# Kernel optimization log

Measured on AMD Instinct MI355X. Metric: run time of the kernel, lower is better.

Reference implementation:

```python
import jax, jax.numpy as jnp
import numpy as np

H = W = 32
C = 512
RED = 16


def make_gus(v=1.5):
    # gus[p=(i,k), x, y] = exp(-((x-i)^2+(y-k)^2)/(2 v^2)) / (2 pi v^2), normalized per p.
    idx = np.arange(H, dtype=np.float64)
    d2 = (idx[:, None] - idx[None, :]) ** 2          # [center, coord]
    g1 = np.exp(-d2 / (2.0 * v * v))                  # separable factor
    g = np.einsum('ix,ky->ikxy', g1, g1) / (2.0 * np.pi * v * v)
    g = g / g.sum(axis=(2, 3), keepdims=True)         # per-position normalization
    return jnp.asarray(g.reshape(H * W, H, W), dtype=jnp.float32)


def setup_inputs() -> dict:
    key = jax.random.key(0)
    ks = jax.random.split(key, 6)
    b = 16
    return {
        'x': jax.random.normal(ks[0], (b, C, H, W), dtype=jnp.float32),
        'se_w1': jax.random.normal(ks[1], (C // RED, C), dtype=jnp.float32) * 0.02,
        'se_b1': jnp.zeros((C // RED,), dtype=jnp.float32),
        'se_w2': jax.random.normal(ks[2], (C, C // RED), dtype=jnp.float32) * 0.02,
        'se_b2': jnp.zeros((C,), dtype=jnp.float32),
        'down_w': jax.random.normal(ks[3], (C, 2 * C), dtype=jnp.float32) * 0.02,
        'gus': make_gus(1.5),
    }


def _patches3(img, h, w):
    # img: [b, c, h+2, w+2] -> [b, c, h, w, 9] (3x3 neighborhoods, row-major dy*3+dx)
    ps = [img[:, :, dy:dy + h, dx:dx + w] for dy in range(3) for dx in range(3)]
    return jnp.stack(ps, axis=-1)


def reference(x, se_w1, se_b1, se_w2, se_b2, down_w, gus):
    b, c, h, w = x.shape
    # --- SELayer ---
    s = x.mean(axis=(2, 3))                                   # [b, c]
    y = jax.nn.relu(s @ se_w1.T + se_b1)                       # [b, c/16]
    y = jax.nn.sigmoid(y @ se_w2.T + se_b2)                    # [b, c]
    out32 = x * y[:, :, None, None]
    # --- gaussian-weighted global pooling per output position ---
    # g[b, p, ch] = sum_{y,x} gus[p,y,x] * out32[b,ch,y,x]; then torch's view(c,h,w)
    gus_out = jnp.einsum('pyx,bcyx->bpc', gus, out32).reshape(b, c, h, w)
    # --- patch self-attention ---
    sig = jax.nn.sigmoid(out32)
    sigp = _patches3(jnp.pad(sig, ((0, 0), (0, 0), (1, 1), (1, 1))), h, w)    # [b,c,h,w,9]
    ffp = _patches3(jnp.pad(out32, ((0, 0), (0, 0), (1, 1), (1, 1))), h, w)   # [b,c,h,w,9]
    logits = jnp.einsum('bcyx,bcyxk->byxk', sig, sigp) / c     # mean over channels
    attn = jax.nn.softmax(logits, axis=-1)                     # softmax over 3x3 patch
    g2 = jnp.einsum('byxk,bcyxk->byxc', attn, ffp)             # [b,h,w,c] = [b, p, c]
    out_csa = g2.reshape(b, c, h, w)                           # torch view(c,h,w) of [hw,c]
    # --- down: 1x1 conv (no bias) + InstanceNorm2d + LeakyReLU(0.2) ---
    cat = jnp.concatenate([gus_out, out_csa], axis=1)          # [b, 2c, h, w]
    z = jnp.einsum('oi,biyx->boyx', down_w, cat)
    mu = z.mean(axis=(2, 3), keepdims=True)
    var = z.var(axis=(2, 3), keepdims=True)
    zn = (z - mu) * jax.lax.rsqrt(var + 1e-5)
    return jnp.where(zn >= 0, zn, 0.2 * zn)
```

## Files before the change

### kernel.cpp

```cpp
#include <hip/hip_runtime.h>
#include <stdint.h>

#define NB 16
#define NC 512
#define NS 1024
#define NR 32

typedef unsigned short u16;
typedef unsigned int u32;

typedef __attribute__((ext_vector_type(8))) short short8;
typedef __attribute__((ext_vector_type(4))) float f32x4;

__device__ __forceinline__ float bf2f(u16 u) {
    union { u32 i; float f; } c; c.i = ((u32)u) << 16; return c.f;
}
__device__ __forceinline__ u16 f2bf(float f) {
    union { float f; u32 i; } c; c.f = f;
    u32 r = (c.i + 0x7FFFu + ((c.i >> 16) & 1u)) >> 16;
    return (u16)r;
}
__device__ __forceinline__ float sigm(float x) {
    return 1.0f / (1.0f + __expf(-x));
}

#define GLD16(gp, lp)                                                      \
    __builtin_amdgcn_global_load_lds(                                      \
        (const __attribute__((address_space(1))) u32*)(gp),                \
        (__attribute__((address_space(3))) u32*)(lp), 16, 0, 0)

__global__ void k_pre(const float* __restrict__ x, float* __restrict__ sm,
                      const float* __restrict__ dw, u16* __restrict__ dwb,
                      const float* __restrict__ g, u16* __restrict__ gt) {
    __shared__ __align__(16) float shb[64 * 65];
    const int t = threadIdx.x;
    if (blockIdx.x < NB * NC) {
        const int row = blockIdx.x;
        const float4* xr = (const float4*)(x + (long)row * NS);
        float4 v = xr[t];
        float p = v.x + v.y + v.z + v.w;
        for (int off = 32; off; off >>= 1) p += __shfl_down(p, off);
        if ((t & 63) == 0) shb[t >> 6] = p;
        __syncthreads();
        if (t == 0) sm[row] = (shb[0] + shb[1] + shb[2] + shb[3]) * (1.0f / 1024.0f);
    } else if (blockIdx.x < NB * NC + 2048) {
        const int i = (blockIdx.x - NB * NC) * 256 + t;
        dwb[i] = f2bf(dw[i]);
    } else {
        const int gbx = blockIdx.x - (NB * NC + 2048);
        const int p0 = (gbx & 15) * 64;
        const int k0 = (gbx >> 4) * 64;
        float (*tile)[65] = (float(*)[65])shb;
#pragma unroll
        for (int it = 0; it < 4; ++it) {
            int c = it * 256 + t;
            int row = c >> 4;
            int f4 = c & 15;
            float4 v = *(const float4*)&g[(long)(p0 + row) * 1024 + k0 + f4 * 4];
            tile[row][f4 * 4 + 0] = v.x; tile[row][f4 * 4 + 1] = v.y;
            tile[row][f4 * 4 + 2] = v.z; tile[row][f4 * 4 + 3] = v.w;
        }
        __syncthreads();
        const int q = t >> 7, k_loc = t & 63, h = (t >> 6) & 1;
        short8 v0, v1;
#pragma unroll
        for (int jj = 0; jj < 8; ++jj) {
            v0[jj] = (short)f2bf(tile[2 * (h * 16 + jj) + q][k_loc]);
            v1[jj] = (short)f2bf(tile[2 * (h * 16 + 8 + jj) + q][k_loc]);
        }
        long ob = (long)q * 524288 + (long)(k0 + k_loc) * 512 + (p0 >> 1) + h * 16;
        *(short8*)&gt[ob] = v0;
        *(short8*)&gt[ob + 8] = v1;
    }
}

#define MFMA_TILE_STEP(As, Bs, NW)                                                  \
    {                                                                               \
        _Pragma("unroll")                                                           \
        for (int kk = 0; kk < 128; kk += 32) {                                      \
            const int gq = (kk >> 3) + (lane >> 4);                                 \
            const int slot = gq ^ (lane & 15);                                      \
            short8 af[4], bfr[NW];                                                  \
            _Pragma("unroll")                                                       \
            for (int i = 0; i < 4; ++i)                                             \
                af[i] = *(const short8*)&As[(wm + i * 16 + (lane & 15)) * 128 + slot * 8]; \
            _Pragma("unroll")                                                       \
            for (int j = 0; j < NW; ++j)                                            \
                bfr[j] = *(const short8*)&Bs[(wn + j * 16 + (lane & 15)) * 128 + slot * 8]; \
            _Pragma("unroll")                                                       \
            for (int i = 0; i < 4; ++i)                                             \
                _Pragma("unroll")                                                   \
                for (int j = 0; j < NW; ++j)                                        \
                    acc[i][j] = __builtin_amdgcn_mfma_f32_16x16x32_bf16(af[i], bfr[j], acc[i][j], 0, 0, 0); \
        }                                                                           \
    }

__global__ __launch_bounds__(256)
void k_we(const u16* __restrict__ dwb, const u16* __restrict__ gt,
          u16* __restrict__ Eb, const float* __restrict__ sm,
          const float* __restrict__ w1, const float* __restrict__ b1,
          const float* __restrict__ w2, const float* __restrict__ b2,
          float* __restrict__ y) {
    __shared__ __align__(16) u16 As[128 * 128];
    __shared__ __align__(16) u16 Bs[128 * 128];
    const int bx = blockIdx.x;
    const int tid = threadIdx.x;
    if (bx < 64) {
        const int q = bx >> 5, rem = bx & 31;
        const int m0 = (rem >> 3) * 128, n0 = (rem & 7) * 128;
        const u16* Bb = gt + (long)q * 524288;
        const int lane = tid & 63, wave = tid >> 6;
        const int wm = (wave >> 1) * 64, wn = (wave & 1) * 64;
        f32x4 acc[4][4];
#pragma unroll
        for (int i = 0; i < 4; ++i)
#pragma unroll
            for (int j = 0; j < 4; ++j) acc[i][j] = (f32x4){0.f, 0.f, 0.f, 0.f};
        int srow[8], sg8[8];
#pragma unroll
        for (int r = 0; r < 8; ++r) {
            int c = r * 256 + tid;
            srow[r] = c >> 4;
            sg8[r] = ((c & 15) ^ (srow[r] & 15)) * 8;
        }
        for (int k0 = 0; k0 < 512; k0 += 128) {
#pragma unroll
            for (int r = 0; r < 8; ++r) {
                const int c = r * 256 + tid;
                GLD16(dwb + (long)(m0 + srow[r]) * 1024 + (k0 + sg8[r]), &As[c * 8]);
                GLD16(Bb + (long)(n0 + srow[r]) * 512 + (k0 + sg8[r]), &Bs[c * 8]);
            }
            __syncthreads();
            MFMA_TILE_STEP(As, Bs, 4);
            __syncthreads();
        }
        const int col = lane & 15, rq = (lane >> 4) * 4;
#pragma unroll
        for (int i = 0; i < 4; ++i)
#pragma unroll
            for (int j = 0; j < 4; ++j)
#pragma unroll
                for (int r = 0; r < 4; ++r) {
                    int row = m0 + wm + i * 16 + rq + r;
                    int ncol = n0 + wn + j * 16 + col;
                    Eb[(long)q * 524288 + (long)row * 1024 + ncol] = f2bf(acc[i][j][r]);
                }
    } else {
        const int b = bx - 64;
        float* s_s = (float*)As;
        float* s_y1 = (float*)Bs;
        const int t = tid;
        s_s[t] = sm[b * NC + t];
        s_s[t + 256] = sm[b * NC + t + 256];
        __syncthreads();
        {
            const int r = t >> 3, sub = t & 7;
            const float4* wr = (const float4*)(w1 + r * NC + sub * 64);
            const float4* sv = (const float4*)(s_s + sub * 64);
            float acc = 0.f;
#pragma unroll
            for (int i = 0; i < 16; ++i) {
                float4 wv = wr[i];
                float4 s4 = sv[i];
                acc += wv.x * s4.x + wv.y * s4.y + wv.z * s4.z + wv.w * s4.w;
            }
            acc += __shfl_down(acc, 4);
            acc += __shfl_down(acc, 2);
            acc += __shfl_down(acc, 1);
            if (sub == 0) s_y1[r] = fmaxf(acc + b1[r], 0.0f);
        }
        __syncthreads();
        for (int i = 0; i < 2; ++i) {
            int c = t + i * 256;
            float acc = b2[c];
#pragma unroll
            for (int r = 0; r < NR; ++r) acc += s_y1[r] * w2[c * NR + r];
            y[b * NC + c] = 1.0f / (1.0f + expf(-acc));
        }
    }
}

__global__ void k_scale(const float* __restrict__ x, const float* __restrict__ y,
                        u16* __restrict__ o32, u16* __restrict__ o32t,
                        u16* __restrict__ sig_t) {
    const int b = blockIdx.z;
    const int c0 = blockIdx.y * 32;
    const int s0 = blockIdx.x * 32;
    const int tx = threadIdx.x & 31, ty = threadIdx.x >> 5;
    __shared__ float tile[32][33];
    const float* xb = x + (long)b * NC * NS;
#pragma unroll
    for (int it = 0; it < 4; ++it) {
        int c = c0 + ty + it * 8;
        float v = xb[(long)c * NS + s0 + tx] * y[b * NC + c];
        tile[ty + it * 8][tx] = v;
        o32[((long)b * NC + c) * NS + s0 + tx] = f2bf(v);
    }
    __syncthreads();
#pragma unroll
    for (int it = 0; it < 4; ++it) {
        int sr = ty + it * 8;
        float tv = tile[tx][sr];
        long idx = ((long)b * NS + (s0 + sr)) * NC + c0 + tx;
        o32t[idx] = f2bf(tv);
        if (sig_t) sig_t[idx] = f2bf(sigm(tv));
    }
}

template <bool ONFLY>
__global__ __launch_bounds__(512)
void k_attn(const u16* __restrict__ sig_t, const u16* __restrict__ o32t,
            u16* __restrict__ g2) {
    const int wave = threadIdx.x >> 6, lane = threadIdx.x & 63;
    const int tid = threadIdx.x;
    const int bx = blockIdx.x;
    const int b = blockIdx.y;
    const int y0 = bx >> 2;
    const int xbase = (bx & 3) * 8;
    const long base = (long)b * NS * NC;
    __shared__ __align__(16) u16 smem[2 * 30 * NC];

#pragma unroll
    for (int it = 0; it < 4; ++it) {
        int idx = it * 512 + tid;
        if (idx < 30 * 64) {
            int pair = idx >> 6;
            int ch0 = (idx & 63) * 8;
            int prow = pair / 10;
            int pxc = pair - prow * 10;
            int yy = y0 + prow - 1;
            int xx = xbase + pxc - 1;
            short8 rv = (short8){0, 0, 0, 0, 0, 0, 0, 0};
            short8 sv = (short8){0, 0, 0, 0, 0, 0, 0, 0};
            if (yy >= 0 && yy < 32 && xx >= 0 && xx < 32) {
                long roff = base + (long)(yy * 32 + xx) * NC + ch0;
                rv = *(const short8*)&o32t[roff];
                if (ONFLY) {
#pragma unroll
                    for (int j = 0; j < 8; ++j) sv[j] = (short)f2bf(sigm(bf2f((u16)rv[j])));
                } else {
                    sv = *(const short8*)&sig_t[roff];
                }
            }
            *(short8*)&smem[pair * NC + ch0] = sv;
            *(short8*)&smem[(30 + pair) * NC + ch0] = rv;
        }
    }
    __syncthreads();

    const int coff = lane * 8;
    short8 csv = *(const short8*)&smem[(11 + wave) * NC + coff];
    float sc[8];
#pragma unroll
    for (int j = 0; j < 8; ++j) sc[j] = bf2f((u16)csv[j]);

    float part[9];
#pragma unroll
    for (int k = 0; k < 9; ++k) {
        int pair = (k / 3) * 10 + wave + k % 3;
        short8 sv = *(const short8*)&smem[pair * NC + coff];
        float p = 0.f;
#pragma unroll
        for (int j = 0; j < 8; ++j) p += sc[j] * bf2f((u16)sv[j]);
        part[k] = p;
    }
#pragma unroll
    for (int k = 0; k < 9; ++k)
        for (int off = 32; off; off >>= 1) part[k] += __shfl_down(part[k], off);

    if (lane == 0) {
        float mx = -1e30f;
#pragma unroll
        for (int k = 0; k < 9; ++k) { part[k] *= (1.0f / 512.0f); mx = fmaxf(mx, part[k]); }
        float sum = 0.f;
#pragma unroll
        for (int k = 0; k < 9; ++k) { part[k] = __expf(part[k] - mx); sum += part[k]; }
        float inv = 1.0f / sum;
#pragma unroll
        for (int k = 0; k < 9; ++k) part[k] *= inv;
    }
    float g[8] = {0.f, 0.f, 0.f, 0.f, 0.f, 0.f, 0.f, 0.f};
#pragma unroll
    for (int k = 0; k < 9; ++k) {
        float a = __shfl(part[k], 0);
        int pair = (k / 3) * 10 + wave + k % 3;
        short8 rv = *(const short8*)&smem[(30 + pair) * NC + coff];
#pragma unroll
        for (int j = 0; j < 8; ++j) g[j] += a * bf2f((u16)rv[j]);
    }
    short8 ov;
#pragma unroll
    for (int j = 0; j < 8; ++j) ov[j] = (short)f2bf(g[j]);
    const int s = y0 * 32 + xbase + wave;
    *(short8*)&g2[base + (long)s * NC + coff] = ov;
}

__global__ __launch_bounds__(256)
void k_tr2(const u16* __restrict__ g2, u16* __restrict__ gs) {
    const int b = blockIdx.y;
    const int c0 = (blockIdx.x & 7) * 64;
    const int j0 = ((blockIdx.x >> 3) & 7) * 64;
    const int q = blockIdx.x >> 6;
    const int t = threadIdx.x;
    __shared__ __align__(16) u16 tile[64 * 64];
    const u16* src = g2 + (long)b * 524288 + (long)(2 * j0 + q) * 512 + c0;
#pragma unroll
    for (int it = 0; it < 2; ++it) {
        int c = it * 256 + t;
        int jl = c >> 3, sg = c & 7;
        short8 v = *(const short8*)&src[(long)jl * 1024 + sg * 8];
        int slot = sg ^ ((jl >> 3) & 7);
        *(short8*)&tile[jl * 64 + slot * 8] = v;
    }
    __syncthreads();
#pragma unroll
    for (int it = 0; it < 2; ++it) {
        int c = it * 256 + t;
        int cl = c >> 3, jg = c & 7;
        const int gcs = cl >> 3, co = cl & 7;
        short8 v;
#pragma unroll
        for (int jj = 0; jj < 8; ++jj) {
            int j = jg * 8 + jj;
            int slot = gcs ^ jg;
            v[jj] = (short)tile[j * 64 + slot * 8 + co];
        }
        *(short8*)&gs[(long)b * 524288 + (long)q * 262144 +
                      (long)(c0 + cl) * 512 + j0 + jg * 8] = v;
    }
}

__global__ __launch_bounds__(512)
void k_zgemm(const u16* __restrict__ Em, const u16* __restrict__ dwb,
             const u16* __restrict__ o32, const u16* __restrict__ gsep,
             u16* __restrict__ Z) {
    const int b = blockIdx.z;
    const int band = blockIdx.y & 1;
    const int m0 = (blockIdx.y >> 1) * 128;
    const int n0 = blockIdx.x * 128;
    __shared__ __align__(16) u16 As[128 * 128];
    __shared__ __align__(16) u16 Bs[128 * 128];
    const int tid = threadIdx.x;
    const int lane = tid & 63, wave = tid >> 6;
    const int wm = (wave >> 2) * 64, wn = (wave & 3) * 32;
    f32x4 acc[4][2];
#pragma unroll
    for (int i = 0; i < 4; ++i)
#pragma unroll
        for (int j = 0; j < 2; ++j) acc[i][j] = (f32x4){0.f, 0.f, 0.f, 0.f};

    const u16* A0 = Em + (long)band * 524288 + (long)m0 * 1024;
    const u16* B0 = o32 + (long)b * 524288 + (long)n0 * 1024;
    const u16* A1 = dwb + 512 + (long)m0 * 1024;
    const u16* B1 = gsep + (long)b * 524288 + (long)band * 262144 + (long)n0 * 512;

#define ZSTAGE(k0, Abase, Bbase, ldb)                                         \
    {                                                                         \
        _Pragma("unroll")                                                     \
        for (int r = 0; r < 4; ++r) {                                         \
            const int c = r * 512 + tid;                                      \
            const int srow = c >> 4;                                          \
            const int sg = ((c & 15) ^ (srow & 15)) * 8;                      \
            GLD16((Abase) + (long)srow * 1024 + (k0 + sg), &As[c * 8]);       \
            GLD16((Bbase) + (long)srow * (ldb) + (k0 + sg), &Bs[c * 8]);      \
        }                                                                     \
    }

    for (int k0 = 0; k0 < 1024; k0 += 128) {
        ZSTAGE(k0, A0, B0, 1024);
        __syncthreads();
        MFMA_TILE_STEP(As, Bs, 2);
        __syncthreads();
    }
    for (int k0 = 0; k0 < 512; k0 += 128) {
        ZSTAGE(k0, A1, B1, 512);
        __syncthreads();
        MFMA_TILE_STEP(As, Bs, 2);
        __syncthreads();
    }
#undef ZSTAGE
    const int col = lane & 15, rq = (lane >> 4) * 4;
#pragma unroll
    for (int i = 0; i < 4; ++i)
#pragma unroll
        for (int j = 0; j < 2; ++j)
#pragma unroll
            for (int r = 0; r < 4; ++r) {
                int row = m0 + wm + i * 16 + rq + r;
                int ncol = n0 + wn + j * 16 + col;
                Z[((long)b * 512 + row) * 1024 + band * 512 + ncol] = f2bf(acc[i][j][r]);
            }
}

__global__ void k_norm(const u16* __restrict__ z, float* __restrict__ out) {
    const int row = blockIdx.x;
    const int t = threadIdx.x;
    uint2 u = ((const uint2*)(z + (long)row * NS))[t];
    float v0 = bf2f((u16)(u.x & 0xffffu)), v1 = bf2f((u16)(u.x >> 16));
    float v2 = bf2f((u16)(u.y & 0xffffu)), v3 = bf2f((u16)(u.y >> 16));
    float sm = v0 + v1 + v2 + v3;
    float sq = v0 * v0 + v1 * v1 + v2 * v2 + v3 * v3;
    for (int off = 32; off; off >>= 1) { sm += __shfl_down(sm, off); sq += __shfl_down(sq, off); }
    __shared__ __align__(16) float rs[4], rq2[4];
    if ((t & 63) == 0) { rs[t >> 6] = sm; rq2[t >> 6] = sq; }
    __syncthreads();
    float tot = rs[0] + rs[1] + rs[2] + rs[3];
    float totq = rq2[0] + rq2[1] + rq2[2] + rq2[3];
    float mu = tot * (1.0f / 1024.0f);
    float var = totq * (1.0f / 1024.0f) - mu * mu;
    float sc = rsqrtf(var + 1e-5f);
    float4 o;
    float a;
    a = (v0 - mu) * sc; o.x = (a >= 0.f) ? a : 0.2f * a;
    a = (v1 - mu) * sc; o.y = (a >= 0.f) ? a : 0.2f * a;
    a = (v2 - mu) * sc; o.z = (a >= 0.f) ? a : 0.2f * a;
    a = (v3 - mu) * sc; o.w = (a >= 0.f) ? a : 0.2f * a;
    ((float4*)(out + (long)row * NS))[t] = o;
}

extern "C" void kernel_launch(void* const* d_in, const int* in_sizes, int n_in,
                              void* d_out, int out_size, void* d_ws, size_t ws_size,
                              hipStream_t stream) {
    const float* x   = (const float*)d_in[0];
    const float* w1  = (const float*)d_in[1];
    const float* b1  = (const float*)d_in[2];
    const float* w2  = (const float*)d_in[3];
    const float* b2  = (const float*)d_in[4];
    const float* dw  = (const float*)d_in[5];
    const float* gus = (const float*)d_in[6];
    float* out = (float*)d_out;
    char* ws = (char*)d_ws;

    float* sm_buf = (float*)(ws + 0);
    float* y_buf  = (float*)(ws + 32768);
    u16* dwbf     = (u16*)(ws + 65536);
    u16* gusTb    = (u16*)(ws + 1114112);
    u16* Ebuf     = (u16*)(ws + 3211264);
    u16* o32      = (u16*)(ws + 5308416);
    u16* o32t     = (u16*)(ws + 22085632);
    const bool big = (ws_size >= 72417280UL);
    u16* sig_t    = big ? (u16*)(ws + 38862848) : (u16*)0;
    u16* g2b      = big ? (u16*)(ws + 55640064) : (u16*)(ws + 38862848);
    u16* g2sep    = (u16*)(ws + 22085632);
    u16* Z        = g2b;

    k_pre<<<dim3(NB * NC + 2048 + 256), dim3(256), 0, stream>>>(
        x, sm_buf, dw, dwbf, gus, gusTb);
    k_we<<<dim3(80), dim3(256), 0, stream>>>(
        dwbf, gusTb, Ebuf, sm_buf, w1, b1, w2, b2, y_buf);
    k_scale<<<dim3(32, 16, NB), dim3(256), 0, stream>>>(x, y_buf, o32, o32t, sig_t);
    if (big)
        k_attn<false><<<dim3(128, NB), dim3(512), 0, stream>>>(sig_t, o32t, g2b);
    else
        k_attn<true><<<dim3(128, NB), dim3(512), 0, stream>>>(sig_t, o32t, g2b);
    k_tr2<<<dim3(128, NB), dim3(256), 0, stream>>>(g2b, g2sep);
    k_zgemm<<<dim3(4, 8, NB), dim3(512), 0, stream>>>(Ebuf, dwbf, o32, g2sep, Z);
    k_norm<<<dim3(NB * NC), dim3(256), 0, stream>>>(Z, out);
}
```

Before: 185.7 us.

## Double-buffer k_zgemm shared tiles with 64-wide K stages

```diff
diff --git a/kernel.cpp b/kernel.cpp
--- a/kernel.cpp
+++ b/kernel.cpp
@@ -95,6 +95,27 @@
         }                                                                           \
     }
 
+#define MFMA_TILE_STEP64(As, Bs)                                                    \
+    {                                                                               \
+        _Pragma("unroll")                                                           \
+        for (int kk = 0; kk < 64; kk += 32) {                                       \
+            const int gq = (kk >> 3) + (lane >> 4);                                 \
+            const int slot = gq ^ (lane & 7);                                       \
+            short8 af[4], bfr[2];                                                   \
+            _Pragma("unroll")                                                       \
+            for (int i = 0; i < 4; ++i)                                             \
+                af[i] = *(const short8*)&As[(wm + i * 16 + (lane & 15)) * 64 + slot * 8]; \
+            _Pragma("unroll")                                                       \
+            for (int j = 0; j < 2; ++j)                                             \
+                bfr[j] = *(const short8*)&Bs[(wn + j * 16 + (lane & 15)) * 64 + slot * 8]; \
+            _Pragma("unroll")                                                       \
+            for (int i = 0; i < 4; ++i)                                             \
+                _Pragma("unroll")                                                   \
+                for (int j = 0; j < 2; ++j)                                         \
+                    acc[i][j] = __builtin_amdgcn_mfma_f32_16x16x32_bf16(af[i], bfr[j], acc[i][j], 0, 0, 0); \
+        }                                                                           \
+    }
+
 __global__ __launch_bounds__(256)
 void k_we(const u16* __restrict__ dwb, const u16* __restrict__ gt,
           u16* __restrict__ Eb, const float* __restrict__ sm,
@@ -338,8 +359,8 @@
     const int band = blockIdx.y & 1;
     const int m0 = (blockIdx.y >> 1) * 128;
     const int n0 = blockIdx.x * 128;
-    __shared__ __align__(16) u16 As[128 * 128];
-    __shared__ __align__(16) u16 Bs[128 * 128];
+    __shared__ __align__(16) u16 As[2][128 * 64];
+    __shared__ __align__(16) u16 Bs[2][128 * 64];
     const int tid = threadIdx.x;
     const int lane = tid & 63, wave = tid >> 6;
     const int wm = (wave >> 2) * 64, wn = (wave & 3) * 32;
@@ -354,31 +375,32 @@
     const u16* A1 = dwb + 512 + (long)m0 * 1024;
     const u16* B1 = gsep + (long)b * 524288 + (long)band * 262144 + (long)n0 * 512;
 
-#define ZSTAGE(k0, Abase, Bbase, ldb)                                         \
+#define ZSTAGE64(tt, bi)                                                      \
     {                                                                         \
+        const int k0_ = (tt) * 64;                                            \
+        const u16* Ab_;                                                       \
+        const u16* Bb_;                                                       \
+        long ldb_;                                                            \
+        if (k0_ < 1024) { Ab_ = A0 + k0_; Bb_ = B0 + k0_; ldb_ = 1024; }      \
+        else { Ab_ = A1 + (k0_ - 1024); Bb_ = B1 + (k0_ - 1024); ldb_ = 512; }\
         _Pragma("unroll")                                                     \
-        for (int r = 0; r < 4; ++r) {                                         \
+        for (int r = 0; r < 2; ++r) {                                         \
             const int c = r * 512 + tid;                                      \
-            const int srow = c >> 4;                                          \
-            const int sg = ((c & 15) ^ (srow & 15)) * 8;                      \
-            GLD16((Abase) + (long)srow * 1024 + (k0 + sg), &As[c * 8]);       \
-            GLD16((Bbase) + (long)srow * (ldb) + (k0 + sg), &Bs[c * 8]);      \
+            const int srow = c >> 3;                                          \
+            const int sg = ((c & 7) ^ (srow & 7)) * 8;                        \
+            GLD16(Ab_ + (long)srow * 1024 + sg, &As[bi][c * 8]);              \
+            GLD16(Bb_ + (long)srow * ldb_ + sg, &Bs[bi][c * 8]);              \
         }                                                                     \
     }
 
-    for (int k0 = 0; k0 < 1024; k0 += 128) {
-        ZSTAGE(k0, A0, B0, 1024);
+    ZSTAGE64(0, 0);
+    __syncthreads();
+    for (int t = 0; t < 24; ++t) {
+        if (t < 23) ZSTAGE64(t + 1, (t + 1) & 1);
+        MFMA_TILE_STEP64(As[t & 1], Bs[t & 1]);
         __syncthreads();
-        MFMA_TILE_STEP(As, Bs, 2);
-        __syncthreads();
-    }
-    for (int k0 = 0; k0 < 512; k0 += 128) {
-        ZSTAGE(k0, A1, B1, 512);
-        __syncthreads();
-        MFMA_TILE_STEP(As, Bs, 2);
-        __syncthreads();
-    }
-#undef ZSTAGE
+    }
+#undef ZSTAGE64
     const int col = lane & 15, rq = (lane >> 4) * 4;
 #pragma unroll
     for (int i = 0; i < 4; ++i)
```

Result: no change. 187.0 us (+0.7%).
